# Kernel tuning notes

Measured on AMD Instinct MI355X. Metric: run time of the kernel, lower is better.

Reference implementation:

```python
import jax, jax.numpy as jnp
import numpy as np


def _pairwise_dist(src, dst):
    # src: [B,K,3,M], dst: [B,K,3,N] -> Euclidean distances [B,K,M,N]
    sq_src = jnp.sum(src * src, axis=2)            # [B,K,M]
    sq_dst = jnp.sum(dst * dst, axis=2)            # [B,K,N]
    cross = jnp.einsum('bkcm,bkcn->bkmn', src, dst)  # [B,K,M,N]
    d2 = sq_src[..., :, None] + sq_dst[..., None, :] - 2.0 * cross
    return jnp.sqrt(jnp.maximum(d2, 0.0))


def setup_inputs() -> dict:
    key = jax.random.key(0)
    k1, k2 = jax.random.split(key)
    B, K, M, N = 16, 8, 1024, 1024
    part_pc_src_input = jax.random.normal(k1, (B, K, 3, M), dtype=jnp.float32)
    part_pc_dst_input = jax.random.normal(k2, (B, K, 3, N), dtype=jnp.float32)
    return {"part_pc_src_input": part_pc_src_input,
            "part_pc_dst_input": part_pc_dst_input}


def reference(part_pc_src_input, part_pc_dst_input):
    # dist[b,k,m,n] = ||src[b,k,:,m] - dst[b,k,:,n]||_2
    dist = _pairwise_dist(part_pc_src_input, part_pc_dst_input)
    # forward: min over dst points, mean over (batch, src points) -> per part [K]
    forward_loss = jnp.min(dist, axis=3).mean(axis=(0, 2))
    # backward: min over src points, mean over (batch, dst points) -> per part [K]
    backward_loss = jnp.min(dist, axis=2).mean(axis=(0, 2))
    chamfer_per_part = forward_loss + backward_loss  # [K]
    return jnp.mean(chamfer_per_part)
```

## Files before the change

### kernel.cpp

```cpp
#include <hip/hip_runtime.h>


#define NPTS 1024
#define TPB 1024
#define NSPLIT 8
#define QPT 8
#define TGT (NPTS / NSPLIT)

__global__ __launch_bounds__(TPB) void chamfer_onepass_kernel(
    const float* __restrict__ src,
    const float* __restrict__ dst,
    float* __restrict__ out, int BK, float scale) {
  __shared__ float4 tgt[NPTS];
  __shared__ unsigned cmb[NPTS];
  __shared__ float wsum[2];

  const int t = threadIdx.x;
  const int pair = blockIdx.x;
  const int dir = pair >= BK;
  const int bk = dir ? (pair - BK) : pair;
  const float* A = (dir ? dst : src) + (size_t)bk * 3 * NPTS;
  const float* Bb = (dir ? src : dst) + (size_t)bk * 3 * NPTS;

  {
    float x = Bb[t], y = Bb[NPTS + t], z = Bb[2 * NPTS + t];
    tgt[t] = make_float4(x, y, z, fmaf(x, x, fmaf(y, y, z * z)));
    cmb[t] = 0x7F800000u;
  }
  __syncthreads();

  const int qg = t & 127;
  const int split = t >> 7;

  float ax[QPT], ay[QPT], az[QPT], sq[QPT], mn[QPT];
#pragma unroll
  for (int j = 0; j < QPT; ++j) {
    const int m = qg + j * 128;
    float x = A[m], y = A[NPTS + m], z = A[2 * NPTS + m];
    ax[j] = -2.0f * x;
    ay[j] = -2.0f * y;
    az[j] = -2.0f * z;
    sq[j] = fmaf(x, x, fmaf(y, y, z * z));
    mn[j] = 3.4e38f;
  }

  const float4* ts = &tgt[split * TGT];
#pragma unroll 8
  for (int n = 0; n < TGT; ++n) {
    float4 d = ts[n];
#pragma unroll
    for (int j = 0; j < QPT; ++j) {
      float v = fmaf(ax[j], d.x, fmaf(ay[j], d.y, fmaf(az[j], d.z, d.w)));
      mn[j] = fminf(mn[j], v);
    }
  }

#pragma unroll
  for (int j = 0; j < QPT; ++j) {
    float m = fmaxf(sq[j] + mn[j], 0.0f);
    atomicMin(&cmb[j * 128 + qg], __float_as_uint(m));
  }
  __syncthreads();

  if (t < 128) {
    float v = 0.0f;
#pragma unroll
    for (int j = 0; j < QPT; ++j)
      v += sqrtf(__uint_as_float(cmb[j * 128 + t]));
    for (int off = 32; off > 0; off >>= 1) v += __shfl_down(v, off);
    if ((t & 63) == 0) wsum[t >> 6] = v;
  }
  __syncthreads();
  if (t == 0) atomicAdd(out, (wsum[0] + wsum[1]) * scale);
}

extern "C" void kernel_launch(void* const* d_in, const int* in_sizes, int n_in,
                              void* d_out, int out_size, void* d_ws, size_t ws_size,
                              hipStream_t stream) {
  const float* src = (const float*)d_in[0];
  const float* dst = (const float*)d_in[1];
  float* out = (float*)d_out;

  const int BK = in_sizes[0] / (3 * NPTS);
  const float scale = 1.0f / (float)(BK * NPTS);

  hipMemsetAsync(out, 0, sizeof(float), stream);

  dim3 grid(2 * BK);
  chamfer_onepass_kernel<<<grid, TPB, 0, stream>>>(src, dst, out, BK, scale);
}
```

Baseline: 78.86 us.

## Pack query pairs into float2 FMAs and replace the atomic sum with a final-reduce kernel

The inner distance loop now handles queries in pairs as two-wide float vectors, so the compiler can emit packed FP32 FMA instructions and issue fewer FMA instructions per target point. The minimum step stays scalar. The memset and global atomicAdd are replaced by per-block partial sums in workspace, followed by a small second kernel that reduces them. This trades one memset and contended atomics for an extra kernel launch, and the summation order becomes deterministic. With 2*BK = 256 blocks, the final kernel's 256 threads cover every partial sum only if BK is at most 128.

```diff
diff --git a/kernel.cpp b/kernel.cpp
--- a/kernel.cpp
+++ b/kernel.cpp
@@ -1,16 +1,20 @@
 #include <hip/hip_runtime.h>
 
+
+typedef float v2f __attribute__((ext_vector_type(2)));
 
 #define NPTS 1024
 #define TPB 1024
 #define NSPLIT 8
 #define QPT 8
+#define QP2 (QPT / 2)
 #define TGT (NPTS / NSPLIT)
 
-__global__ __launch_bounds__(TPB) void chamfer_onepass_kernel(
+__global__ __launch_bounds__(TPB) void chamfer_main_kernel(
     const float* __restrict__ src,
     const float* __restrict__ dst,
-    float* __restrict__ out, int BK, float scale) {
+    float* __restrict__ part,
+    int BK) {
   __shared__ float4 tgt[NPTS];
   __shared__ unsigned cmb[NPTS];
   __shared__ float wsum[2];
@@ -32,33 +36,41 @@
   const int qg = t & 127;
   const int split = t >> 7;
 
-  float ax[QPT], ay[QPT], az[QPT], sq[QPT], mn[QPT];
+  v2f ax[QP2], ay[QP2], az[QP2], sq[QP2], mn[QP2];
 #pragma unroll
-  for (int j = 0; j < QPT; ++j) {
-    const int m = qg + j * 128;
-    float x = A[m], y = A[NPTS + m], z = A[2 * NPTS + m];
-    ax[j] = -2.0f * x;
-    ay[j] = -2.0f * y;
-    az[j] = -2.0f * z;
-    sq[j] = fmaf(x, x, fmaf(y, y, z * z));
-    mn[j] = 3.4e38f;
+  for (int p = 0; p < QP2; ++p) {
+    const int m0 = qg + (2 * p) * 128, m1 = qg + (2 * p + 1) * 128;
+    float x0 = A[m0], y0 = A[NPTS + m0], z0 = A[2 * NPTS + m0];
+    float x1 = A[m1], y1 = A[NPTS + m1], z1 = A[2 * NPTS + m1];
+    ax[p] = (v2f){-2.0f * x0, -2.0f * x1};
+    ay[p] = (v2f){-2.0f * y0, -2.0f * y1};
+    az[p] = (v2f){-2.0f * z0, -2.0f * z1};
+    sq[p] = (v2f){fmaf(x0, x0, fmaf(y0, y0, z0 * z0)),
+                  fmaf(x1, x1, fmaf(y1, y1, z1 * z1))};
+    mn[p] = (v2f){3.4e38f, 3.4e38f};
   }
 
   const float4* ts = &tgt[split * TGT];
 #pragma unroll 8
   for (int n = 0; n < TGT; ++n) {
     float4 d = ts[n];
+    v2f dx = {d.x, d.x}, dy = {d.y, d.y}, dz = {d.z, d.z}, dw = {d.w, d.w};
 #pragma unroll
-    for (int j = 0; j < QPT; ++j) {
-      float v = fmaf(ax[j], d.x, fmaf(ay[j], d.y, fmaf(az[j], d.z, d.w)));
-      mn[j] = fminf(mn[j], v);
+    for (int p = 0; p < QP2; ++p) {
+      v2f v = __builtin_elementwise_fma(az[p], dz, dw);
+      v = __builtin_elementwise_fma(ay[p], dy, v);
+      v = __builtin_elementwise_fma(ax[p], dx, v);
+      mn[p].x = fminf(mn[p].x, v.x);
+      mn[p].y = fminf(mn[p].y, v.y);
     }
   }
 
 #pragma unroll
-  for (int j = 0; j < QPT; ++j) {
-    float m = fmaxf(sq[j] + mn[j], 0.0f);
-    atomicMin(&cmb[j * 128 + qg], __float_as_uint(m));
+  for (int p = 0; p < QP2; ++p) {
+    v2f m2 = sq[p] + mn[p];
+    float a = fmaxf(m2.x, 0.0f), b = fmaxf(m2.y, 0.0f);
+    atomicMin(&cmb[(2 * p) * 128 + qg], __float_as_uint(a));
+    atomicMin(&cmb[(2 * p + 1) * 128 + qg], __float_as_uint(b));
   }
   __syncthreads();
 
@@ -71,7 +83,19 @@
     if ((t & 63) == 0) wsum[t >> 6] = v;
   }
   __syncthreads();
-  if (t == 0) atomicAdd(out, (wsum[0] + wsum[1]) * scale);
+  if (t == 0) part[pair] = wsum[0] + wsum[1];
+}
+
+__global__ __launch_bounds__(256) void chamfer_final_kernel(
+    const float* __restrict__ part, float* __restrict__ out, int n,
+    float scale) {
+  const int t = threadIdx.x;
+  float v = (t < n) ? part[t] : 0.0f;
+  for (int off = 32; off > 0; off >>= 1) v += __shfl_down(v, off);
+  __shared__ float wsum[4];
+  if ((t & 63) == 0) wsum[t >> 6] = v;
+  __syncthreads();
+  if (t == 0) out[0] = (wsum[0] + wsum[1] + wsum[2] + wsum[3]) * scale;
 }
 
 extern "C" void kernel_launch(void* const* d_in, const int* in_sizes, int n_in,
@@ -80,12 +104,12 @@
   const float* src = (const float*)d_in[0];
   const float* dst = (const float*)d_in[1];
   float* out = (float*)d_out;
+  float* part = (float*)d_ws;
 
   const int BK = in_sizes[0] / (3 * NPTS);
   const float scale = 1.0f / (float)(BK * NPTS);
 
-  hipMemsetAsync(out, 0, sizeof(float), stream);
-
   dim3 grid(2 * BK);
-  chamfer_onepass_kernel<<<grid, TPB, 0, stream>>>(src, dst, out, BK, scale);
+  chamfer_main_kernel<<<grid, TPB, 0, stream>>>(src, dst, part, BK);
+  chamfer_final_kernel<<<1, 256, 0, stream>>>(part, out, 2 * BK, scale);
 }
```

New measurement: 76.97 us. -2.4%, faster.

## Use packed FP32 FMA over target pairs and replace atomic sum with final reduce kernel

Applied to the files above, without the earlier changes.

The inner distance loop now handles two target points at a time, using v_pk_fma_f32 on a shared-memory layout that interleaves pairs of targets (x0,x1,y0,y1 / z0,z1,w0,w1). The aim is to halve the FMA instruction count per query-target pair. The global atomicAdd and the memset are replaced by per-block partial sums written to workspace, followed by a small second kernel that reduces them. The min operations remain scalar, so the gain is limited to the FMA part, and the extra kernel launch adds some overhead.

```diff
diff --git a/kernel.cpp b/kernel.cpp
--- a/kernel.cpp
+++ b/kernel.cpp
@@ -1,16 +1,26 @@
 #include <hip/hip_runtime.h>
 
+
+typedef float v2f __attribute__((ext_vector_type(2)));
 
 #define NPTS 1024
 #define TPB 1024
 #define NSPLIT 8
 #define QPT 8
 #define TGT (NPTS / NSPLIT)
+#define PAIRS (TGT / 2)
 
-__global__ __launch_bounds__(TPB) void chamfer_onepass_kernel(
+__device__ __forceinline__ v2f pk_fma(v2f a, v2f b, v2f c) {
+  v2f d;
+  asm("v_pk_fma_f32 %0, %1, %2, %3" : "=v"(d) : "v"(a), "v"(b), "v"(c));
+  return d;
+}
+
+__global__ __launch_bounds__(TPB) void chamfer_main_kernel(
     const float* __restrict__ src,
     const float* __restrict__ dst,
-    float* __restrict__ out, int BK, float scale) {
+    float* __restrict__ part,
+    int BK) {
   __shared__ float4 tgt[NPTS];
   __shared__ unsigned cmb[NPTS];
   __shared__ float wsum[2];
@@ -22,42 +32,57 @@
   const float* A = (dir ? dst : src) + (size_t)bk * 3 * NPTS;
   const float* Bb = (dir ? src : dst) + (size_t)bk * 3 * NPTS;
 
-  {
-    float x = Bb[t], y = Bb[NPTS + t], z = Bb[2 * NPTS + t];
-    tgt[t] = make_float4(x, y, z, fmaf(x, x, fmaf(y, y, z * z)));
-    cmb[t] = 0x7F800000u;
+  cmb[t] = 0x7F800000u;
+  if (t < NPTS / 2) {
+    const int p = t;
+    float x0 = Bb[2 * p],            x1 = Bb[2 * p + 1];
+    float y0 = Bb[NPTS + 2 * p],     y1 = Bb[NPTS + 2 * p + 1];
+    float z0 = Bb[2 * NPTS + 2 * p], z1 = Bb[2 * NPTS + 2 * p + 1];
+    float w0 = fmaf(x0, x0, fmaf(y0, y0, z0 * z0));
+    float w1 = fmaf(x1, x1, fmaf(y1, y1, z1 * z1));
+    tgt[2 * p]     = make_float4(x0, x1, y0, y1);
+    tgt[2 * p + 1] = make_float4(z0, z1, w0, w1);
   }
   __syncthreads();
 
   const int qg = t & 127;
   const int split = t >> 7;
 
-  float ax[QPT], ay[QPT], az[QPT], sq[QPT], mn[QPT];
+  v2f axp[QPT], ayp[QPT], azp[QPT], mnp[QPT];
+  float sq[QPT];
 #pragma unroll
   for (int j = 0; j < QPT; ++j) {
     const int m = qg + j * 128;
     float x = A[m], y = A[NPTS + m], z = A[2 * NPTS + m];
-    ax[j] = -2.0f * x;
-    ay[j] = -2.0f * y;
-    az[j] = -2.0f * z;
+    float ax = -2.0f * x, ay = -2.0f * y, az = -2.0f * z;
+    axp[j] = (v2f){ax, ax};
+    ayp[j] = (v2f){ay, ay};
+    azp[j] = (v2f){az, az};
     sq[j] = fmaf(x, x, fmaf(y, y, z * z));
-    mn[j] = 3.4e38f;
+    mnp[j] = (v2f){3.4e38f, 3.4e38f};
   }
 
-  const float4* ts = &tgt[split * TGT];
-#pragma unroll 8
-  for (int n = 0; n < TGT; ++n) {
-    float4 d = ts[n];
+  const float4* ts = &tgt[split * 2 * PAIRS];
+#pragma unroll 4
+  for (int p = 0; p < PAIRS; ++p) {
+    float4 lo = ts[2 * p];
+    float4 hi = ts[2 * p + 1];
+    v2f xx = {lo.x, lo.y}, yy = {lo.z, lo.w};
+    v2f zz = {hi.x, hi.y}, ww = {hi.z, hi.w};
 #pragma unroll
     for (int j = 0; j < QPT; ++j) {
-      float v = fmaf(ax[j], d.x, fmaf(ay[j], d.y, fmaf(az[j], d.z, d.w)));
-      mn[j] = fminf(mn[j], v);
+      v2f v = pk_fma(azp[j], zz, ww);
+      v = pk_fma(ayp[j], yy, v);
+      v = pk_fma(axp[j], xx, v);
+      mnp[j].x = fminf(mnp[j].x, v.x);
+      mnp[j].y = fminf(mnp[j].y, v.y);
     }
   }
 
 #pragma unroll
   for (int j = 0; j < QPT; ++j) {
-    float m = fmaxf(sq[j] + mn[j], 0.0f);
+    float m = sq[j] + fminf(mnp[j].x, mnp[j].y);
+    m = fmaxf(m, 0.0f);
     atomicMin(&cmb[j * 128 + qg], __float_as_uint(m));
   }
   __syncthreads();
@@ -71,7 +96,19 @@
     if ((t & 63) == 0) wsum[t >> 6] = v;
   }
   __syncthreads();
-  if (t == 0) atomicAdd(out, (wsum[0] + wsum[1]) * scale);
+  if (t == 0) part[pair] = wsum[0] + wsum[1];
+}
+
+__global__ __launch_bounds__(256) void chamfer_final_kernel(
+    const float* __restrict__ part, float* __restrict__ out, int n,
+    float scale) {
+  const int t = threadIdx.x;
+  float v = (t < n) ? part[t] : 0.0f;
+  for (int off = 32; off > 0; off >>= 1) v += __shfl_down(v, off);
+  __shared__ float wsum[4];
+  if ((t & 63) == 0) wsum[t >> 6] = v;
+  __syncthreads();
+  if (t == 0) out[0] = (wsum[0] + wsum[1] + wsum[2] + wsum[3]) * scale;
 }
 
 extern "C" void kernel_launch(void* const* d_in, const int* in_sizes, int n_in,
@@ -80,12 +117,12 @@
   const float* src = (const float*)d_in[0];
   const float* dst = (const float*)d_in[1];
   float* out = (float*)d_out;
+  float* partbuf = (float*)d_ws;
 
   const int BK = in_sizes[0] / (3 * NPTS);
   const float scale = 1.0f / (float)(BK * NPTS);
 
-  hipMemsetAsync(out, 0, sizeof(float), stream);
-
   dim3 grid(2 * BK);
-  chamfer_onepass_kernel<<<grid, TPB, 0, stream>>>(src, dst, out, BK, scale);
+  chamfer_main_kernel<<<grid, TPB, 0, stream>>>(src, dst, partbuf, BK);
+  chamfer_final_kernel<<<1, 256, 0, stream>>>(partbuf, out, 2 * BK, scale);
 }
```

Measured after the change: 78.71 us. About the same (-0.2%).

## Compute each distance tile once for both directions with packed FMA

Applied to the files above, without the earlier changes.

The two-direction pass (one block per direction per part) becomes a single tiled kernel. Each distance tile is computed once and feeds both the row minima (forward) and the column minima (backward). Column minima go to a global workspace through atomicMin, and a second single-block kernel does the sqrt and the sum. The inner loop uses v_pk_fma_f32 and v_min3_f32 through inline asm, which halves the distance arithmetic and cuts instruction count. In exchange the change adds a workspace memset, global atomics, cross-lane shuffles and an extra kernel launch. The 0xFF memset initialises colmin to NaN bit patterns, which are larger than any positive float when compared as unsigned, so it serves as the min identity.

```diff
diff --git a/kernel.cpp b/kernel.cpp
--- a/kernel.cpp
+++ b/kernel.cpp
@@ -1,77 +1,146 @@
 #include <hip/hip_runtime.h>
 
 
+typedef float v2f __attribute__((ext_vector_type(2)));
+
 #define NPTS 1024
-#define TPB 1024
-#define NSPLIT 8
-#define QPT 8
-#define TGT (NPTS / NSPLIT)
+#define ROWS 128
+#define TPB 256
+#define RM 8
+#define NCHUNK 4
+#define QPC 8
 
-__global__ __launch_bounds__(TPB) void chamfer_onepass_kernel(
-    const float* __restrict__ src,
-    const float* __restrict__ dst,
-    float* __restrict__ out, int BK, float scale) {
-  __shared__ float4 tgt[NPTS];
-  __shared__ unsigned cmb[NPTS];
-  __shared__ float wsum[2];
+__device__ __forceinline__ v2f pk_fma(v2f a, v2f b, v2f c) {
+  v2f d;
+  asm("v_pk_fma_f32 %0, %1, %2, %3" : "=v"(d) : "v"(a), "v"(b), "v"(c));
+  return d;
+}
+__device__ __forceinline__ float min3f(float a, float b, float c) {
+  float d;
+  asm("v_min3_f32 %0, %1, %2, %3" : "=v"(d) : "v"(a), "v"(b), "v"(c));
+  return d;
+}
+
+__global__ __launch_bounds__(TPB, 4) void chamfer_tile_kernel(
+    const float* __restrict__ src, const float* __restrict__ dst,
+    unsigned* __restrict__ colmin,
+    float* __restrict__ rowsum,
+    int BK) {
+  __shared__ float4 rowq[ROWS];
+  __shared__ float4 colqA[NPTS / 2];
+  __shared__ float4 colqB[NPTS / 2];
+  __shared__ float wred[4];
 
   const int t = threadIdx.x;
-  const int pair = blockIdx.x;
-  const int dir = pair >= BK;
-  const int bk = dir ? (pair - BK) : pair;
-  const float* A = (dir ? dst : src) + (size_t)bk * 3 * NPTS;
-  const float* Bb = (dir ? src : dst) + (size_t)bk * 3 * NPTS;
+  const int bk = blockIdx.x >> 3;
+  const int rb = blockIdx.x & 7;
+  const float* S = src + (size_t)bk * 3 * NPTS;
+  const float* D = dst + (size_t)bk * 3 * NPTS;
 
-  {
-    float x = Bb[t], y = Bb[NPTS + t], z = Bb[2 * NPTS + t];
-    tgt[t] = make_float4(x, y, z, fmaf(x, x, fmaf(y, y, z * z)));
-    cmb[t] = 0x7F800000u;
+  if (t < ROWS) {
+    int m = rb * ROWS + t;
+    float x = S[m], y = S[NPTS + m], z = S[2 * NPTS + m];
+    rowq[t] = make_float4(-2.f * x, -2.f * y, -2.f * z,
+                          fmaf(x, x, fmaf(y, y, z * z)));
+  }
+  for (int p = t; p < NPTS / 2; p += TPB) {
+    float x0 = D[2 * p],            x1 = D[2 * p + 1];
+    float y0 = D[NPTS + 2 * p],     y1 = D[NPTS + 2 * p + 1];
+    float z0 = D[2 * NPTS + 2 * p], z1 = D[2 * NPTS + 2 * p + 1];
+    colqA[p] = make_float4(x0, x1, y0, y1);
+    colqB[p] = make_float4(z0, z1, fmaf(x0, x0, fmaf(y0, y0, z0 * z0)),
+                                   fmaf(x1, x1, fmaf(y1, y1, z1 * z1)));
   }
   __syncthreads();
 
-  const int qg = t & 127;
-  const int split = t >> 7;
+  const int c = t & 15;
+  const int r = t >> 4;
 
-  float ax[QPT], ay[QPT], az[QPT], sq[QPT], mn[QPT];
+  v2f rxp[RM], ryp[RM], rzp[RM], sqp[RM];
+  float rmn[RM];
 #pragma unroll
-  for (int j = 0; j < QPT; ++j) {
-    const int m = qg + j * 128;
-    float x = A[m], y = A[NPTS + m], z = A[2 * NPTS + m];
-    ax[j] = -2.0f * x;
-    ay[j] = -2.0f * y;
-    az[j] = -2.0f * z;
-    sq[j] = fmaf(x, x, fmaf(y, y, z * z));
-    mn[j] = 3.4e38f;
+  for (int i = 0; i < RM; ++i) {
+    float4 q = rowq[r * RM + i];
+    rxp[i] = (v2f){q.x, q.x};
+    ryp[i] = (v2f){q.y, q.y};
+    rzp[i] = (v2f){q.z, q.z};
+    sqp[i] = (v2f){q.w, q.w};
+    rmn[i] = 3.4e38f;
   }
 
-  const float4* ts = &tgt[split * TGT];
-#pragma unroll 8
-  for (int n = 0; n < TGT; ++n) {
-    float4 d = ts[n];
+  for (int k = 0; k < NCHUNK; ++k) {
+    v2f cm[QPC];
 #pragma unroll
-    for (int j = 0; j < QPT; ++j) {
-      float v = fmaf(ax[j], d.x, fmaf(ay[j], d.y, fmaf(az[j], d.z, d.w)));
-      mn[j] = fminf(mn[j], v);
+    for (int q = 0; q < QPC; ++q) cm[q] = (v2f){3.4e38f, 3.4e38f};
+
+#pragma unroll
+    for (int q = 0; q < QPC; ++q) {
+      const int P = k * 128 + q * 16 + c;
+      float4 A = colqA[P];
+      float4 B = colqB[P];
+      v2f xx = {A.x, A.y}, yy = {A.z, A.w};
+      v2f zz = {B.x, B.y}, ss = {B.z, B.w};
+#pragma unroll
+      for (int i = 0; i < RM; ++i) {
+        v2f v = pk_fma(rzp[i], zz, ss);
+        v = pk_fma(ryp[i], yy, v);
+        v = pk_fma(rxp[i], xx, v);
+        rmn[i] = min3f(rmn[i], v.x, v.y);
+        v2f cv = v + sqp[i];
+        cm[q].x = fminf(cm[q].x, cv.x);
+        cm[q].y = fminf(cm[q].y, cv.y);
+      }
+    }
+#pragma unroll
+    for (int q = 0; q < QPC; ++q) {
+      float a = cm[q].x, b = cm[q].y;
+      a = fminf(a, __shfl_xor(a, 16)); a = fminf(a, __shfl_xor(a, 32));
+      b = fminf(b, __shfl_xor(b, 16)); b = fminf(b, __shfl_xor(b, 32));
+      if (((t >> 4) & 3) == 0) {
+        const int P = k * 128 + q * 16 + c;
+        atomicMin(&colmin[bk * NPTS + 2 * P],
+                  __float_as_uint(fmaxf(a, 0.f)));
+        atomicMin(&colmin[bk * NPTS + 2 * P + 1],
+                  __float_as_uint(fmaxf(b, 0.f)));
+      }
     }
   }
 
+  float rsum = 0.f;
 #pragma unroll
-  for (int j = 0; j < QPT; ++j) {
-    float m = fmaxf(sq[j] + mn[j], 0.0f);
-    atomicMin(&cmb[j * 128 + qg], __float_as_uint(m));
+  for (int i = 0; i < RM; ++i) {
+    float a = rmn[i];
+    a = fminf(a, __shfl_xor(a, 1));
+    a = fminf(a, __shfl_xor(a, 2));
+    a = fminf(a, __shfl_xor(a, 4));
+    a = fminf(a, __shfl_xor(a, 8));
+    rsum += sqrtf(fmaxf(sqp[i].x + a, 0.f));
   }
+  float v = (c == 0) ? rsum : 0.f;
+  for (int off = 32; off; off >>= 1) v += __shfl_down(v, off);
+  if ((t & 63) == 0) wred[t >> 6] = v;
   __syncthreads();
+  if (t == 0) rowsum[blockIdx.x] = wred[0] + wred[1] + wred[2] + wred[3];
+}
 
-  if (t < 128) {
-    float v = 0.0f;
+__global__ __launch_bounds__(1024) void chamfer_reduce_kernel(
+    const unsigned* __restrict__ colmin, const float* __restrict__ rowsum,
+    float* __restrict__ out, int BK, float scale) {
+  const int t = threadIdx.x;
+  float s = rowsum[t];
+  const int CN = BK * NPTS;
+  for (int j = t; j < CN; j += 1024)
+    s += sqrtf(__uint_as_float(colmin[j]));
+  for (int off = 32; off; off >>= 1) s += __shfl_down(s, off);
+  __shared__ float wr[16];
+  if ((t & 63) == 0) wr[t >> 6] = s;
+  __syncthreads();
+  if (t == 0) {
+    float tot = 0.f;
 #pragma unroll
-    for (int j = 0; j < QPT; ++j)
-      v += sqrtf(__uint_as_float(cmb[j * 128 + t]));
-    for (int off = 32; off > 0; off >>= 1) v += __shfl_down(v, off);
-    if ((t & 63) == 0) wsum[t >> 6] = v;
+    for (int w = 0; w < 16; ++w) tot += wr[w];
+    out[0] = tot * scale;
   }
-  __syncthreads();
-  if (t == 0) atomicAdd(out, (wsum[0] + wsum[1]) * scale);
 }
 
 extern "C" void kernel_launch(void* const* d_in, const int* in_sizes, int n_in,
@@ -84,8 +153,13 @@
   const int BK = in_sizes[0] / (3 * NPTS);
   const float scale = 1.0f / (float)(BK * NPTS);
 
-  hipMemsetAsync(out, 0, sizeof(float), stream);
+  unsigned* colmin = (unsigned*)d_ws;
+  float* rowsum = (float*)((char*)d_ws + (size_t)BK * NPTS * 4);
 
-  dim3 grid(2 * BK);
-  chamfer_onepass_kernel<<<grid, TPB, 0, stream>>>(src, dst, out, BK, scale);
+  hipMemsetAsync(colmin, 0xFF, (size_t)BK * NPTS * 4, stream);
+
+  dim3 grid1(BK * 8);
+  chamfer_tile_kernel<<<grid1, TPB, 0, stream>>>(src, dst, colmin, rowsum, BK);
+
+  chamfer_reduce_kernel<<<1, 1024, 0, stream>>>(colmin, rowsum, out, BK, scale);
 }
```

Measured after the change: 216.7 us. +174.9%, slower.
